# Kernel tuning notes

Measured on AMD Instinct MI355X. Metric: run time of the kernel, lower is better.

Reference implementation:

```python
import jax, jax.numpy as jnp
import numpy as np

# regular 3x3 kernel grid: row0 = dy (i-1), row1 = dx (j-1), k = 3*i + j
RY = jnp.array([-1., -1., -1., 0., 0., 0., 1., 1., 1.], dtype=jnp.float32)
RX = jnp.array([-1., 0., 1., -1., 0., 1., -1., 0., 1.], dtype=jnp.float32)


def conv2d(x, w, b):
    # 3x3, stride 1, pad 1, NCHW/OIHW
    out = jax.lax.conv_general_dilated(
        x, w, window_strides=(1, 1), padding=((1, 1), (1, 1)),
        dimension_numbers=('NCHW', 'OIHW', 'NCHW'))
    return out + b[None, :, None, None]


def group_norm(x, gamma, beta, num_groups, eps=1e-5):
    N, C, H, W = x.shape
    xg = x.reshape(N, num_groups, C // num_groups, H, W)
    mu = xg.mean(axis=(2, 3, 4), keepdims=True)
    var = xg.var(axis=(2, 3, 4), keepdims=True)
    xn = ((xg - mu) * jax.lax.rsqrt(var + eps)).reshape(N, C, H, W)
    return xn * gamma[None, :, None, None] + beta[None, :, None, None]


def build_offset(tm, tr):
    # tm: [N,4,H,W] per-pixel 2x2 affine [[m00,m01],[m10,m11]]; tr: [N,2,H,W] (ty, tx)
    m00, m01, m10, m11 = tm[:, 0], tm[:, 1], tm[:, 2], tm[:, 3]  # [N,H,W]
    ry = RY[None, :, None, None]
    rx = RX[None, :, None, None]
    # offset = M @ R - R, plus translation broadcast to all 9 points
    dy = m00[:, None] * ry + m01[:, None] * rx - ry + tr[:, 0:1]  # [N,9,H,W]
    dx = m10[:, None] * ry + m11[:, None] * rx - rx + tr[:, 1:2]  # [N,9,H,W]
    return dy, dx


def bilinear_sample(img, py, px):
    # img: [N,C,H,W]; py, px: [N,K,H,W] sampling locations; zero padding outside
    N, C, H, W = img.shape
    K = py.shape[1]
    y0f = jnp.floor(py)
    x0f = jnp.floor(px)
    wy1 = py - y0f
    wx1 = px - x0f
    wy0 = 1.0 - wy1
    wx0 = 1.0 - wx1
    y0 = y0f.astype(jnp.int32)
    x0 = x0f.astype(jnp.int32)
    img_flat = img.reshape(N, C, H * W)

    def gather(yi, xi):
        valid = ((yi >= 0) & (yi < H) & (xi >= 0) & (xi < W)).astype(img.dtype)
        idx = jnp.clip(yi, 0, H - 1) * W + jnp.clip(xi, 0, W - 1)  # [N,K,H,W]
        flat = idx.reshape(N, 1, K * H * W)
        vals = jnp.take_along_axis(img_flat, jnp.broadcast_to(flat, (N, C, K * H * W)), axis=2)
        return vals.reshape(N, C, K, H, W) * valid[:, None]

    v00 = gather(y0, x0)
    v01 = gather(y0, x0 + 1)
    v10 = gather(y0 + 1, x0)
    v11 = gather(y0 + 1, x0 + 1)
    return (v00 * (wy0 * wx0)[:, None] + v01 * (wy0 * wx1)[:, None]
            + v10 * (wy1 * wx0)[:, None] + v11 * (wy1 * wx1)[:, None])


def deform_conv(x, dy, dx, w, pad=1, dil=1):
    # x: [N,Cin,H,W]; dy,dx: [N,9,H,W]; w: [Cout,Cin,3,3]; stride 1
    N, C, H, W = x.shape
    k = jnp.arange(9)
    ki = (k // 3).astype(x.dtype)[None, :, None, None]
    kj = (k % 3).astype(x.dtype)[None, :, None, None]
    hh = jnp.arange(H, dtype=x.dtype)[None, None, :, None]
    ww = jnp.arange(W, dtype=x.dtype)[None, None, None, :]
    py = hh - pad + dil * ki + dy  # [N,9,H,W]
    px = ww - pad + dil * kj + dx
    sampled = bilinear_sample(x, py, px)  # [N,C,9,H,W]
    return jnp.einsum('nckhw,ock->nohw', sampled, w.reshape(w.shape[0], C, 9))


def setup_inputs() -> dict:
    key = jax.random.key(0)
    ks = jax.random.split(key, 16)
    N, C, H, W = 4, 256, 64, 64
    x = jax.random.normal(ks[0], (N, C, H, W), jnp.float32)
    def p(k, shape, s):
        return jax.random.normal(k, shape, jnp.float32) * s
    s_off = 0.01                       # small STN heads -> modest offsets
    s_dc = 1.0 / np.sqrt(C * 9.0)      # deform-conv fan-in init
    return {
        'x': x,
        'w_tm1': p(ks[1], (4, C, 3, 3), s_off), 'b_tm1': jnp.zeros((4,), jnp.float32),
        'w_tr1': p(ks[2], (2, C, 3, 3), s_off), 'b_tr1': jnp.zeros((2,), jnp.float32),
        'w_dc1': p(ks[3], (C, C, 3, 3), s_dc),
        'g1': jnp.ones((C,), jnp.float32), 'be1': jnp.zeros((C,), jnp.float32),
        'w_tm2': p(ks[4], (4, C, 3, 3), s_off), 'b_tm2': jnp.zeros((4,), jnp.float32),
        'w_tr2': p(ks[5], (2, C, 3, 3), s_off), 'b_tr2': jnp.zeros((2,), jnp.float32),
        'w_dc2': p(ks[6], (C, C, 3, 3), s_dc),
        'g2': jnp.ones((C,), jnp.float32), 'be2': jnp.zeros((C,), jnp.float32),
    }


def reference(x, w_tm1, b_tm1, w_tr1, b_tr1, w_dc1, g1, be1,
              w_tm2, b_tm2, w_tr2, b_tr2, w_dc2, g2, be2):
    GROUPS = 32
    residual = x
    dy1, dx1 = build_offset(conv2d(x, w_tm1, b_tm1), conv2d(x, w_tr1, b_tr1))
    out = deform_conv(x, dy1, dx1, w_dc1)
    out = jax.nn.relu(group_norm(out, g1, be1, GROUPS))
    dy2, dx2 = build_offset(conv2d(out, w_tm2, b_tm2), conv2d(out, w_tr2, b_tr2))
    out = deform_conv(out, dy2, dx2, w_dc2)
    out = group_norm(out, g2, be2, GROUPS)
    return jax.nn.relu(out + residual)
```

## Files before the change

### kernel.cpp

```cpp
#include <hip/hip_runtime.h>


typedef unsigned int u32;
typedef unsigned short u16;
typedef __attribute__((ext_vector_type(8))) short bf16x8;
typedef __attribute__((ext_vector_type(4))) float floatx4;

#define HW 4096
#define CHW 1048576

static __device__ __forceinline__ float bf2f(u16 u) {
    union { u32 i; float f; } c; c.i = ((u32)u) << 16; return c.f;
}
static __device__ __forceinline__ u16 f2bf(float f) {
    union { float f; u32 i; } c; c.f = f;
    u32 x = c.i;
    return (u16)((x + 0x7FFFu + ((x >> 16) & 1u)) >> 16);
}
static __device__ __forceinline__ u32 cvtpk(float a, float b) {
    u32 r;
    asm("v_cvt_pk_bf16_f32 %0, %1, %2" : "=v"(r) : "v"(a), "v"(b));
    return r;
}
static __device__ __forceinline__ void lbar() {
    __builtin_amdgcn_sched_barrier(0);
    asm volatile("s_waitcnt lgkmcnt(0)" ::: "memory");
    __builtin_amdgcn_s_barrier();
    __builtin_amdgcn_sched_barrier(0);
}
static __device__ __forceinline__ float loadv(const void* p, long i, int f32) {
    return f32 ? ((const float*)p)[i] : bf2f(((const u16*)p)[i]);
}
static __device__ __forceinline__ int sniff_f32(const u32* __restrict__ xw) {
    int cnt = 0;
    #pragma unroll
    for (int s = 0; s < 16; ++s) {
        union { u32 i; float f; } c;
        c.i = xw[s * 131 + 7];
        float a = fabsf(c.f);
        if (a > 1e-8f && a < 1e4f) ++cnt;
    }
    return (cnt >= 8) ? 1 : 0;
}

__global__ __launch_bounds__(256) void k_prep_all(
    const void* __restrict__ x,
    const void* __restrict__ wdc1, const void* __restrict__ wdc2,
    const void* __restrict__ wtm1, const void* __restrict__ wtr1,
    const void* __restrict__ wtm2, const void* __restrict__ wtr2,
    u16* __restrict__ xT, u16* __restrict__ wTg1, u16* __restrict__ wTg2,
    u16* __restrict__ wT61, u16* __restrict__ wT62)
{
    __shared__ u16 T[64 * 258];
    const int f32 = sniff_f32((const u32*)x);
    const int b = blockIdx.x;
    const int tid = threadIdx.x;

    if (b < 256) {
        const int n = b >> 6, h = b & 63;
        const long sb = (long)n * CHW + (h << 6);
        const int cb = tid >> 3;
        const int w0 = (tid & 7) << 3;
        if (f32) {
            const float* xp = (const float*)x;
            for (int it = 0; it < 8; ++it) {
                int c = (it << 5) + cb;
                const float* pr = xp + sb + (long)c * HW + w0;
                float4 a = ((const float4*)pr)[0];
                float4 d = ((const float4*)pr)[1];
                T[(w0 + 0) * 258 + c] = f2bf(a.x);
                T[(w0 + 1) * 258 + c] = f2bf(a.y);
                T[(w0 + 2) * 258 + c] = f2bf(a.z);
                T[(w0 + 3) * 258 + c] = f2bf(a.w);
                T[(w0 + 4) * 258 + c] = f2bf(d.x);
                T[(w0 + 5) * 258 + c] = f2bf(d.y);
                T[(w0 + 6) * 258 + c] = f2bf(d.z);
                T[(w0 + 7) * 258 + c] = f2bf(d.w);
            }
        } else {
            const u16* xp = (const u16*)x;
            for (int it = 0; it < 8; ++it) {
                int c = (it << 5) + cb;
                uint4 v = *(const uint4*)(xp + sb + (long)c * HW + w0);
                u32 ws[4] = {v.x, v.y, v.z, v.w};
                #pragma unroll
                for (int q = 0; q < 4; ++q) {
                    T[(w0 + 2 * q + 0) * 258 + c] = (u16)(ws[q] & 0xFFFFu);
                    T[(w0 + 2 * q + 1) * 258 + c] = (u16)(ws[q] >> 16);
                }
            }
        }
        __syncthreads();
        const int w = tid >> 2, cq = tid & 3;
        const u32* Tr = (const u32*)T;
        u16* ob = xT + (long)n * CHW + (long)((h << 6) + w) * 256 + cq * 64;
        #pragma unroll
        for (int s = 0; s < 8; ++s) {
            uint4 o;
            o.x = Tr[129 * w + 32 * cq + 4 * s + 0];
            o.y = Tr[129 * w + 32 * cq + 4 * s + 1];
            o.z = Tr[129 * w + 32 * cq + 4 * s + 2];
            o.w = Tr[129 * w + 32 * cq + 4 * s + 3];
            *(uint4*)&ob[s * 8] = o;
        }
    } else if (b < 2560) {
        const int r2 = (b >= 1408);
        const void* wdc = r2 ? wdc2 : wdc1;
        u16* wTg = r2 ? wTg2 : wTg1;
        int idx2 = (b - (r2 ? 1408 : 256)) * 256 + tid;
        int cp = idx2 & 15;
        int o  = (idx2 >> 4) & 255;
        int q  = idx2 >> 12;
        int k  = q >> 3;
        int c0 = ((q & 7) << 5) + (cp << 1);
        long s0 = (long)o * 2304 + c0 * 9 + k;
        ((u32*)wTg)[idx2] = cvtpk(loadv(wdc, s0, f32), loadv(wdc, s0 + 9, f32));
    } else {
        const int r2 = (b >= 2704);
        const void* wtm = r2 ? wtm2 : wtm1;
        const void* wtr = r2 ? wtr2 : wtr1;
        u16* wT6 = r2 ? wT62 : wT61;
        int i = (b - (r2 ? 2704 : 2560)) * 256 + tid;
        int q  = i >> 9;
        int o  = (i >> 5) & 15;
        int cc = i & 31;
        int k  = q >> 3;
        int c  = ((q & 7) << 5) + cc;
        float v = 0.f;
        if (o < 4)      v = loadv(wtm, (long)o * 2304 + c * 9 + k, f32);
        else if (o < 6) v = loadv(wtr, (long)(o - 4) * 2304 + c * 9 + k, f32);
        wT6[i] = f2bf(v);
    }
}

__global__ __launch_bounds__(512, 4) void k_deform(
    const u16* __restrict__ srcT, const u16* __restrict__ wTg,
    const u16* __restrict__ wT6,
    const void* __restrict__ b_tm, const void* __restrict__ b_tr,
    const u32* __restrict__ xw,
    u16* __restrict__ raw, float* __restrict__ pstats)
{
    __shared__ float red[8][32][17];
    __shared__ float tl[6 * 32];
    __shared__ __align__(16) u32 Sl[2][4096];
    __shared__ int   g_y0[288];
    __shared__ int   g_x0[288];
    __shared__ float g_wy[288];
    __shared__ float g_wx[288];

    const int tid = threadIdx.x;
    const int bid = blockIdx.x;
    const int n = bid >> 7, h = (bid >> 1) & 63, half = bid & 1;
    const int wb = half << 5;
    const int lane = tid & 63;
    const int quad = lane >> 4;
    const int l16  = lane & 15;
    const int wv   = tid >> 6;
    const long nbase = (long)n * CHW;
    const u16* sp = srcT + nbase;

    {
        floatx4 acc6[2];
        acc6[0] = (floatx4){0.f, 0.f, 0.f, 0.f};
        acc6[1] = (floatx4){0.f, 0.f, 0.f, 0.f};
        for (int qi = 0; qi < 9; ++qi) {
            const int q = wv * 9 + qi;
            const int k = q >> 3, cb = q & 7;
            const int ky = k / 3, kx = k % 3;
            const int row = h + ky - 1;
            const bool rv = (row >= 0) && (row < 64);
            bf16x8 av = *(const bf16x8*)&wT6[(((q << 4) + l16) << 5) + (quad << 3)];
            #pragma unroll
            for (int j = 0; j < 2; ++j) {
                int psrc = wb + (j << 4) + l16 + kx - 1;
                bf16x8 bv = {0, 0, 0, 0, 0, 0, 0, 0};
                if (rv && psrc >= 0 && psrc < 64)
                    bv = *(const bf16x8*)&sp[(((long)(row << 6) + psrc) << 8) + (cb << 5) + (quad << 3)];
                acc6[j] = __builtin_amdgcn_mfma_f32_16x16x32_bf16(av, bv, acc6[j], 0, 0, 0);
            }
        }
        #pragma unroll
        for (int j = 0; j < 2; ++j)
            #pragma unroll
            for (int r = 0; r < 4; ++r)
                red[wv][(j << 4) + l16][(quad << 2) + r] = acc6[j][r];
        __syncthreads();
        if (tid < 192) {
            const int o = tid >> 5, px = tid & 31;
            float s = 0.f;
            #pragma unroll
            for (int v = 0; v < 8; ++v) s += red[v][px][o];
            const int f32 = sniff_f32(xw);
            float bias = (o < 4) ? loadv(b_tm, o, f32) : loadv(b_tr, o - 4, f32);
            tl[o * 32 + px] = s + bias;
        }
        __syncthreads();
    }

    for (int i = tid; i < 288; i += 512) {
        int k = i >> 5, ww2 = i & 31;
        float m00 = tl[ww2],       m01 = tl[32 + ww2];
        float m10 = tl[64 + ww2],  m11 = tl[96 + ww2];
        float tr0 = tl[128 + ww2], tr1 = tl[160 + ww2];
        float ry = (float)(k / 3) - 1.f;
        float rx = (float)(k % 3) - 1.f;
        float dy = m00 * ry + m01 * rx - ry + tr0;
        float dx = m10 * ry + m11 * rx - rx + tr1;
        float py = (float)h + ry + dy;
        float px = (float)(wb + ww2) + rx + dx;
        float y0f = floorf(py), x0f = floorf(px);
        g_y0[i] = (int)y0f; g_x0[i] = (int)x0f;
        g_wy[i] = py - y0f; g_wx[i] = px - x0f;
    }
    __syncthreads();

    const int px   = tid >> 4;
    const int slot = tid & 15;
    const int o0   = wv << 5;
    const u32 xw_s = (u32)((px  & 7) << 2);
    const u32 xsw  = (u32)((l16 & 7) << 2);
    const u32 q4x  = (u32)(quad << 2);

    floatx4 acc[2][2];
    #pragma unroll
    for (int i = 0; i < 2; ++i)
        #pragma unroll
        for (int j = 0; j < 2; ++j)
            acc[i][j] = (floatx4){0.f, 0.f, 0.f, 0.f};

    const int wlane = ((o0 + l16) << 5) + (quad << 3);
    const u16* wq = wTg;

    const u16 *p00, *p01, *p10, *p11;
    float cw00, cw01, cw10, cw11;

    auto mkptr = [&](int k) {
        int gi = (k << 5) + px;
        int y0 = g_y0[gi], x0 = g_x0[gi];
        int yc0 = min(max(y0, 0), 63),     yc1 = min(max(y0 + 1, 0), 63);
        int xc0 = min(max(x0, 0), 63),     xc1 = min(max(x0 + 1, 0), 63);
        const u16* bp = sp + (slot << 3);
        p00 = bp + (((yc0 << 6) + xc0) << 8);
        p01 = bp + (((yc0 << 6) + xc1) << 8);
        p10 = bp + (((yc1 << 6) + xc0) << 8);
        p11 = bp + (((yc1 << 6) + xc1) << 8);
    };
    auto mkcw = [&](int k) {
        int gi = (k << 5) + px;
        int y0 = g_y0[gi], x0 = g_x0[gi];
        float wy1 = g_wy[gi], wx1 = g_wx[gi];
        float wy0 = 1.f - wy1, wx0 = 1.f - wx1;
        bool yv0 = (y0 >= 0) && (y0 < 64);
        bool yv1 = (y0 >= -1) && (y0 < 63);
        bool xv0 = (x0 >= 0) && (x0 < 64);
        bool xv1 = (x0 >= -1) && (x0 < 63);
        cw00 = (yv0 && xv0) ? wy0 * wx0 : 0.f;
        cw01 = (yv0 && xv1) ? wy0 * wx1 : 0.f;
        cw10 = (yv1 && xv0) ? wy1 * wx0 : 0.f;
        cw11 = (yv1 && xv1) ? wy1 * wx1 : 0.f;
    };

    uint4 GA, GB, GC, GD, HA, HB, HC, HD;
    auto GATHER = [&]() {
        GA = *(const uint4*)(p00);  HA = *(const uint4*)(p00 + 128);
        GB = *(const uint4*)(p01);  HB = *(const uint4*)(p01 + 128);
        GC = *(const uint4*)(p10);  HC = *(const uint4*)(p10 + 128);
        GD = *(const uint4*)(p11);  HD = *(const uint4*)(p11 + 128);
    };

    bf16x8 W0[4], W1[4];
    auto WLD = [&](int s) {
        W0[s] = *(const bf16x8*)(wq + wlane);
        W1[s] = *(const bf16x8*)(wq + wlane + 512);
        wq += 8192;
    };
    auto MFMA4 = [&](int ws, bf16x8 b0, bf16x8 b1) {
        acc[0][0] = __builtin_amdgcn_mfma_f32_16x16x32_bf16(W0[ws], b0, acc[0][0], 0, 0, 0);
        acc[1][0] = __builtin_amdgcn_mfma_f32_16x16x32_bf16(W1[ws], b0, acc[1][0], 0, 0, 0);
        acc[0][1] = __builtin_amdgcn_mfma_f32_16x16x32_bf16(W0[ws], b1, acc[0][1], 0, 0, 0);
        acc[1][1] = __builtin_amdgcn_mfma_f32_16x16x32_bf16(W1[ws], b1, acc[1][1], 0, 0, 0);
    };

#define BIL(a, b, c, d) cvtpk( \
    fmaf(cw00, bf2f((u16)(a)), fmaf(cw01, bf2f((u16)(b)), \
    fmaf(cw10, bf2f((u16)(c)), cw11 * bf2f((u16)(d))))), \
    fmaf(cw00, bf2f((u16)((a) >> 16)), fmaf(cw01, bf2f((u16)((b) >> 16)), \
    fmaf(cw10, bf2f((u16)((c) >> 16)), cw11 * bf2f((u16)((d) >> 16))))))

    mkptr(0); GATHER();
    WLD(0); WLD(1);

    for (int k = 0; k < 9; ++k) {
        const int buf = k & 1;
        mkcw(k);
        uint4 v0 = make_uint4(BIL(GA.x, GB.x, GC.x, GD.x), BIL(GA.y, GB.y, GC.y, GD.y),
                              BIL(GA.z, GB.z, GC.z, GD.z), BIL(GA.w, GB.w, GC.w, GD.w));
        uint4 v1 = make_uint4(BIL(HA.x, HB.x, HC.x, HD.x), BIL(HA.y, HB.y, HC.y, HD.y),
                              BIL(HA.z, HB.z, HC.z, HD.z), BIL(HA.w, HB.w, HC.w, HD.w));
        u32* wp = &Sl[buf][((u32)(px << 7)) + (((u32)(slot << 2)) ^ xw_s)];
        *(uint4*)wp = v0;
        *(uint4*)(wp + 64) = v1;
        if (k < 8) { mkptr(k + 1); GATHER(); }
        lbar();
        const u32* sb = &Sl[buf][0];
        #pragma unroll
        for (int c = 0; c < 8; ++c) {
            const u32 offc = (((u32)(c << 4)) | q4x) ^ xsw;
            bf16x8 b0 = *(const bf16x8*)(sb + ((u32)(l16 << 7)) + offc);
            bf16x8 b1 = *(const bf16x8*)(sb + ((u32)((16 + l16) << 7)) + offc);
            if (k < 8 || c < 6) WLD((c + 2) & 3);
            MFMA4(c & 3, b0, b1);
        }
    }
#undef BIL

    #pragma unroll
    for (int i = 0; i < 2; ++i) {
        float s1 = 0.f, s2 = 0.f;
        #pragma unroll
        for (int j = 0; j < 2; ++j)
            #pragma unroll
            for (int r = 0; r < 4; ++r) {
                float v = acc[i][j][r];
                s1 += v; s2 += v * v;
            }
        #pragma unroll
        for (int off = 1; off <= 16; off <<= 1) {
            s1 += __shfl_xor(s1, off, 64);
            s2 += __shfl_xor(s2, off, 64);
        }
        if ((lane & 31) == 0) {
            int g = (o0 >> 3) + 2 * i + (lane >> 5);
            pstats[((long)bid << 6) + (g << 1)]     = s1;
            pstats[((long)bid << 6) + (g << 1) + 1] = s2;
        }
    }

    #pragma unroll
    for (int i = 0; i < 2; ++i)
        #pragma unroll
        for (int j = 0; j < 2; ++j)
            #pragma unroll
            for (int r = 0; r < 4; ++r) {
                int o = o0 + i * 16 + quad * 4 + r;
                raw[nbase + ((long)o << 12) + (h << 6) + wb + (j << 4) + l16]
                    = f2bf(acc[i][j][r]);
            }
}

__global__ __launch_bounds__(256) void k_gn_relu(
    const u16* __restrict__ raw, const float* __restrict__ pstats,
    const void* __restrict__ gamma, const void* __restrict__ beta,
    const u32* __restrict__ xw,
    u16* __restrict__ out1)
{
    __shared__ u16 T[64 * 258];
    __shared__ float sred[4][64];
    __shared__ float sl[64];
    const int f32 = sniff_f32(xw);
    const int bid = blockIdx.x;
    const int n = bid >> 6, h = bid & 63;
    const int tid = threadIdx.x;

    {
        const int v = tid & 63, part = tid >> 6;
        float a = 0.f;
        for (int j = part * 32; j < part * 32 + 32; ++j)
            a += pstats[(((long)n * 128 + j) << 6) + v];
        sred[part][v] = a;
        __syncthreads();
        if (tid < 64) sl[tid] = sred[0][tid] + sred[1][tid] + sred[2][tid] + sred[3][tid];
        __syncthreads();
    }

    const u16* rb = raw + (long)n * CHW + (h << 6);
    const int cb = tid >> 3;
    const int w0 = (tid & 7) << 3;
    for (int it = 0; it < 8; ++it) {
        int c = (it << 5) + cb;
        int g = c >> 3;
        float mean = sl[g * 2] * (1.f / 32768.f);
        float var  = sl[g * 2 + 1] * (1.f / 32768.f) - mean * mean;
        float rstd = rsqrtf(var + 1e-5f);
        float ga = loadv(gamma, c, f32) * rstd;
        float be = loadv(beta, c, f32) - mean * ga;
        uint4 v = *(const uint4*)(rb + (long)c * HW + w0);
        u32 ws[4] = {v.x, v.y, v.z, v.w};
        #pragma unroll
        for (int q = 0; q < 4; ++q) {
            float a = fmaxf(fmaf(bf2f((u16)(ws[q] & 0xFFFFu)), ga, be), 0.f);
            float b = fmaxf(fmaf(bf2f((u16)(ws[q] >> 16)),     ga, be), 0.f);
            T[(w0 + 2 * q + 0) * 258 + c] = f2bf(a);
            T[(w0 + 2 * q + 1) * 258 + c] = f2bf(b);
        }
    }
    __syncthreads();
    const int w = tid >> 2, cq = tid & 3;
    const u32* Tr = (const u32*)T;
    u16* ob = out1 + (long)n * CHW + (long)((h << 6) + w) * 256 + cq * 64;
    #pragma unroll
    for (int s = 0; s < 8; ++s) {
        uint4 o;
        o.x = Tr[129 * w + 32 * cq + 4 * s + 0];
        o.y = Tr[129 * w + 32 * cq + 4 * s + 1];
        o.z = Tr[129 * w + 32 * cq + 4 * s + 2];
        o.w = Tr[129 * w + 32 * cq + 4 * s + 3];
        *(uint4*)&ob[s * 8] = o;
    }
}

__global__ __launch_bounds__(256) void k_gn_final(
    const u16* __restrict__ raw, const float* __restrict__ pstats,
    const void* __restrict__ gamma, const void* __restrict__ beta,
    const void* __restrict__ x,
    void* __restrict__ outp)
{
    __shared__ float rr[256];
    const int f32 = sniff_f32((const u32*)x);
    const int tid = threadIdx.x;
    const long e0 = ((long)blockIdx.x) << 11;
    const int n = (int)(e0 >> 20);
    const int c0 = (int)((e0 >> 12) & 255);
    const int g = c0 >> 3;

    {
        int j = tid & 127, sv = tid >> 7;
        rr[tid] = pstats[(((long)n * 128 + j) << 6) + (g << 1) + sv];
        __syncthreads();
        #pragma unroll
        for (int s = 64; s >= 1; s >>= 1) {
            if ((tid & 127) < s) rr[tid] += rr[tid + s];
            __syncthreads();
        }
    }
    float mean = rr[0] * (1.f / 32768.f);
    float var  = rr[128] * (1.f / 32768.f) - mean * mean;
    float rstd = rsqrtf(var + 1e-5f);

    const long i = blockIdx.x * 256 + tid;
    const long e = i << 3;
    const int c = (int)((e >> 12) & 255);
    float ga = loadv(gamma, c, f32) * rstd;
    float be = loadv(beta, c, f32) - mean * ga;
    uint4 p = ((const uint4*)raw)[i];
    u32 ww[4] = {p.x, p.y, p.z, p.w};
    float v[8];
    #pragma unroll
    for (int q = 0; q < 4; ++q) {
        v[2 * q + 0] = fmaxf(fmaf(bf2f((u16)(ww[q] & 0xFFFFu)), ga, be) + loadv(x, e + 2 * q + 0, f32), 0.f);
        v[2 * q + 1] = fmaxf(fmaf(bf2f((u16)(ww[q] >> 16)),     ga, be) + loadv(x, e + 2 * q + 1, f32), 0.f);
    }
    if (f32) {
        float4* op = (float4*)((float*)outp + e);
        op[0] = make_float4(v[0], v[1], v[2], v[3]);
        op[1] = make_float4(v[4], v[5], v[6], v[7]);
    } else {
        uint4 o;
        o.x = cvtpk(v[0], v[1]);
        o.y = cvtpk(v[2], v[3]);
        o.z = cvtpk(v[4], v[5]);
        o.w = cvtpk(v[6], v[7]);
        ((uint4*)outp)[i] = o;
    }
}

extern "C" void kernel_launch(void* const* d_in, const int* in_sizes, int n_in,
                              void* d_out, int out_size, void* d_ws, size_t ws_size,
                              hipStream_t stream) {
    const void* x     = d_in[0];
    const void* w_tm1 = d_in[1];
    const void* b_tm1 = d_in[2];
    const void* w_tr1 = d_in[3];
    const void* b_tr1 = d_in[4];
    const void* w_dc1 = d_in[5];
    const void* g1    = d_in[6];
    const void* be1   = d_in[7];
    const void* w_tm2 = d_in[8];
    const void* b_tm2 = d_in[9];
    const void* w_tr2 = d_in[10];
    const void* b_tr2 = d_in[11];
    const void* w_dc2 = d_in[12];
    const void* g2    = d_in[13];
    const void* be2   = d_in[14];

    char* wsb = (char*)d_ws;
    u16*   xT     = (u16*)wsb;
    u16*   raw    = (u16*)(wsb + 8388608);
    u16*   wTg1   = (u16*)(wsb + 16777216);
    u16*   wTg2   = (u16*)(wsb + 17956864);
    u16*   wT61   = (u16*)(wsb + 19136512);
    u16*   wT62   = (u16*)(wsb + 19210240);
    float* pstats = (float*)(wsb + 19283968);
    u16*   out1   = xT;
    const u32* xw = (const u32*)x;

    k_prep_all<<<2848, 256, 0, stream>>>(x, w_dc1, w_dc2, w_tm1, w_tr1, w_tm2, w_tr2,
                                         xT, wTg1, wTg2, wT61, wT62);
    k_deform  <<<512, 512, 0, stream>>>(xT, wTg1, wT61, b_tm1, b_tr1, xw, raw, pstats);
    k_gn_relu <<<256, 256, 0, stream>>>(raw, pstats, g1, be1, xw, out1);
    k_deform  <<<512, 512, 0, stream>>>(out1, wTg2, wT62, b_tm2, b_tr2, xw, raw, pstats);
    k_gn_final<<<2048, 256, 0, stream>>>(raw, pstats, g2, be2, x, d_out);
}
```

Measured before the change: 239.6 us.

## Process full image rows per deform block with 16 waves instead of half rows

Each deformable-conv block now covers a whole 64-pixel row with 1024 threads (16 waves, 16 output channels each) instead of half a row with 512 threads. The idea is to share the bilinear-gathered tile across more output channels and halve the grid, so offset-conv rows and gathers are not done twice per row. The stats layout shrinks to 64 partials per image and the GN kernels are updated to match. In exchange, shared memory use doubles to about 64 KB, only 256 blocks launch (roughly one per CU), and only 8 of 16 waves take part in the offset conv.

Measured after the change: 221.6 us. 7.5% less time.

```diff
diff --git a/kernel.cpp b/kernel.cpp
--- a/kernel.cpp
+++ b/kernel.cpp
@@ -133,25 +133,23 @@
     }
 }
 
-__global__ __launch_bounds__(512, 4) void k_deform(
+__global__ __launch_bounds__(1024, 4) void k_deform(
     const u16* __restrict__ srcT, const u16* __restrict__ wTg,
     const u16* __restrict__ wT6,
     const void* __restrict__ b_tm, const void* __restrict__ b_tr,
     const u32* __restrict__ xw,
     u16* __restrict__ raw, float* __restrict__ pstats)
 {
-    __shared__ float red[8][32][17];
-    __shared__ float tl[6 * 32];
-    __shared__ __align__(16) u32 Sl[2][4096];
-    __shared__ int   g_y0[288];
-    __shared__ int   g_x0[288];
-    __shared__ float g_wy[288];
-    __shared__ float g_wx[288];
+    __shared__ __align__(16) char shm[65536];
+    __shared__ float tl[6 * 64];
+    __shared__ int   g_y0[576];
+    __shared__ int   g_x0[576];
+    __shared__ float g_wy[576];
+    __shared__ float g_wx[576];
 
     const int tid = threadIdx.x;
     const int bid = blockIdx.x;
-    const int n = bid >> 7, h = (bid >> 1) & 63, half = bid & 1;
-    const int wb = half << 5;
+    const int n = bid >> 6, h = bid & 63;
     const int lane = tid & 63;
     const int quad = lane >> 4;
     const int l16  = lane & 15;
@@ -160,54 +158,58 @@
     const u16* sp = srcT + nbase;
 
     {
-        floatx4 acc6[2];
-        acc6[0] = (floatx4){0.f, 0.f, 0.f, 0.f};
-        acc6[1] = (floatx4){0.f, 0.f, 0.f, 0.f};
-        for (int qi = 0; qi < 9; ++qi) {
-            const int q = wv * 9 + qi;
-            const int k = q >> 3, cb = q & 7;
-            const int ky = k / 3, kx = k % 3;
-            const int row = h + ky - 1;
-            const bool rv = (row >= 0) && (row < 64);
-            bf16x8 av = *(const bf16x8*)&wT6[(((q << 4) + l16) << 5) + (quad << 3)];
+        float (*red)[64][17] = (float (*)[64][17])shm;
+        if (wv < 8) {
+            floatx4 acc6[4];
             #pragma unroll
-            for (int j = 0; j < 2; ++j) {
-                int psrc = wb + (j << 4) + l16 + kx - 1;
-                bf16x8 bv = {0, 0, 0, 0, 0, 0, 0, 0};
-                if (rv && psrc >= 0 && psrc < 64)
-                    bv = *(const bf16x8*)&sp[(((long)(row << 6) + psrc) << 8) + (cb << 5) + (quad << 3)];
-                acc6[j] = __builtin_amdgcn_mfma_f32_16x16x32_bf16(av, bv, acc6[j], 0, 0, 0);
+            for (int j = 0; j < 4; ++j) acc6[j] = (floatx4){0.f, 0.f, 0.f, 0.f};
+            for (int qi = 0; qi < 9; ++qi) {
+                const int q = wv * 9 + qi;
+                const int k = q >> 3, cb = q & 7;
+                const int ky = k / 3, kx = k % 3;
+                const int row = h + ky - 1;
+                const bool rv = (row >= 0) && (row < 64);
+                bf16x8 av = *(const bf16x8*)&wT6[(((q << 4) + l16) << 5) + (quad << 3)];
+                #pragma unroll
+                for (int j = 0; j < 4; ++j) {
+                    int psrc = (j << 4) + l16 + kx - 1;
+                    bf16x8 bv = {0, 0, 0, 0, 0, 0, 0, 0};
+                    if (rv && psrc >= 0 && psrc < 64)
+                        bv = *(const bf16x8*)&sp[(((long)(row << 6) + psrc) << 8) + (cb << 5) + (quad << 3)];
+                    acc6[j] = __builtin_amdgcn_mfma_f32_16x16x32_bf16(av, bv, acc6[j], 0, 0, 0);
+                }
             }
-        }
-        #pragma unroll
-        for (int j = 0; j < 2; ++j)
             #pragma unroll
-            for (int r = 0; r < 4; ++r)
-                red[wv][(j << 4) + l16][(quad << 2) + r] = acc6[j][r];
+            for (int j = 0; j < 4; ++j)
+                #pragma unroll
+                for (int r = 0; r < 4; ++r)
+                    red[wv][(j << 4) + l16][(quad << 2) + r] = acc6[j][r];
+        }
         __syncthreads();
-        if (tid < 192) {
-            const int o = tid >> 5, px = tid & 31;
+        if (tid < 384) {
+            const int o = tid >> 6, px = tid & 63;
             float s = 0.f;
             #pragma unroll
             for (int v = 0; v < 8; ++v) s += red[v][px][o];
             const int f32 = sniff_f32(xw);
             float bias = (o < 4) ? loadv(b_tm, o, f32) : loadv(b_tr, o - 4, f32);
-            tl[o * 32 + px] = s + bias;
+            tl[o * 64 + px] = s + bias;
         }
         __syncthreads();
     }
 
-    for (int i = tid; i < 288; i += 512) {
-        int k = i >> 5, ww2 = i & 31;
-        float m00 = tl[ww2],       m01 = tl[32 + ww2];
-        float m10 = tl[64 + ww2],  m11 = tl[96 + ww2];
-        float tr0 = tl[128 + ww2], tr1 = tl[160 + ww2];
+    if (tid < 576) {
+        int i = tid;
+        int k = i >> 6, ww2 = i & 63;
+        float m00 = tl[ww2],        m01 = tl[64 + ww2];
+        float m10 = tl[128 + ww2],  m11 = tl[192 + ww2];
+        float tr0 = tl[256 + ww2],  tr1 = tl[320 + ww2];
         float ry = (float)(k / 3) - 1.f;
         float rx = (float)(k % 3) - 1.f;
         float dy = m00 * ry + m01 * rx - ry + tr0;
         float dx = m10 * ry + m11 * rx - rx + tr1;
         float py = (float)h + ry + dy;
-        float px = (float)(wb + ww2) + rx + dx;
+        float px = (float)ww2 + rx + dx;
         float y0f = floorf(py), x0f = floorf(px);
         g_y0[i] = (int)y0f; g_x0[i] = (int)x0f;
         g_wy[i] = py - y0f; g_wx[i] = px - x0f;
@@ -216,17 +218,16 @@
 
     const int px   = tid >> 4;
     const int slot = tid & 15;
-    const int o0   = wv << 5;
+    const int o0   = wv << 4;
     const u32 xw_s = (u32)((px  & 7) << 2);
     const u32 xsw  = (u32)((l16 & 7) << 2);
     const u32 q4x  = (u32)(quad << 2);
 
-    floatx4 acc[2][2];
+    u32* Sl = (u32*)shm;
+
+    floatx4 acc[4];
     #pragma unroll
-    for (int i = 0; i < 2; ++i)
-        #pragma unroll
-        for (int j = 0; j < 2; ++j)
-            acc[i][j] = (floatx4){0.f, 0.f, 0.f, 0.f};
+    for (int g = 0; g < 4; ++g) acc[g] = (floatx4){0.f, 0.f, 0.f, 0.f};
 
     const int wlane = ((o0 + l16) << 5) + (quad << 3);
     const u16* wq = wTg;
@@ -235,7 +236,7 @@
     float cw00, cw01, cw10, cw11;
 
     auto mkptr = [&](int k) {
-        int gi = (k << 5) + px;
+        int gi = (k << 6) + px;
         int y0 = g_y0[gi], x0 = g_x0[gi];
         int yc0 = min(max(y0, 0), 63),     yc1 = min(max(y0 + 1, 0), 63);
         int xc0 = min(max(x0, 0), 63),     xc1 = min(max(x0 + 1, 0), 63);
@@ -246,7 +247,7 @@
         p11 = bp + (((yc1 << 6) + xc1) << 8);
     };
     auto mkcw = [&](int k) {
-        int gi = (k << 5) + px;
+        int gi = (k << 6) + px;
         int y0 = g_y0[gi], x0 = g_x0[gi];
         float wy1 = g_wy[gi], wx1 = g_wx[gi];
         float wy0 = 1.f - wy1, wx0 = 1.f - wx1;
@@ -268,17 +269,10 @@
         GD = *(const uint4*)(p11);  HD = *(const uint4*)(p11 + 128);
     };
 
-    bf16x8 W0[4], W1[4];
+    bf16x8 W[4];
     auto WLD = [&](int s) {
-        W0[s] = *(const bf16x8*)(wq + wlane);
-        W1[s] = *(const bf16x8*)(wq + wlane + 512);
+        W[s] = *(const bf16x8*)(wq + wlane);
         wq += 8192;
-    };
-    auto MFMA4 = [&](int ws, bf16x8 b0, bf16x8 b1) {
-        acc[0][0] = __builtin_amdgcn_mfma_f32_16x16x32_bf16(W0[ws], b0, acc[0][0], 0, 0, 0);
-        acc[1][0] = __builtin_amdgcn_mfma_f32_16x16x32_bf16(W1[ws], b0, acc[1][0], 0, 0, 0);
-        acc[0][1] = __builtin_amdgcn_mfma_f32_16x16x32_bf16(W0[ws], b1, acc[0][1], 0, 0, 0);
-        acc[1][1] = __builtin_amdgcn_mfma_f32_16x16x32_bf16(W1[ws], b1, acc[1][1], 0, 0, 0);
     };
 
 #define BIL(a, b, c, d) cvtpk( \
@@ -297,31 +291,36 @@
                               BIL(GA.z, GB.z, GC.z, GD.z), BIL(GA.w, GB.w, GC.w, GD.w));
         uint4 v1 = make_uint4(BIL(HA.x, HB.x, HC.x, HD.x), BIL(HA.y, HB.y, HC.y, HD.y),
                               BIL(HA.z, HB.z, HC.z, HD.z), BIL(HA.w, HB.w, HC.w, HD.w));
-        u32* wp = &Sl[buf][((u32)(px << 7)) + (((u32)(slot << 2)) ^ xw_s)];
+        u32* wp = &Sl[((u32)(buf << 13)) + ((u32)(px << 7)) + (((u32)(slot << 2)) ^ xw_s)];
         *(uint4*)wp = v0;
         *(uint4*)(wp + 64) = v1;
         if (k < 8) { mkptr(k + 1); GATHER(); }
         lbar();
-        const u32* sb = &Sl[buf][0];
+        const u32* sb = &Sl[(u32)(buf << 13)];
         #pragma unroll
         for (int c = 0; c < 8; ++c) {
             const u32 offc = (((u32)(c << 4)) | q4x) ^ xsw;
-            bf16x8 b0 = *(const bf16x8*)(sb + ((u32)(l16 << 7)) + offc);
+            bf16x8 b0 = *(const bf16x8*)(sb + ((u32)(( 0 + l16) << 7)) + offc);
             bf16x8 b1 = *(const bf16x8*)(sb + ((u32)((16 + l16) << 7)) + offc);
+            bf16x8 b2 = *(const bf16x8*)(sb + ((u32)((32 + l16) << 7)) + offc);
+            bf16x8 b3 = *(const bf16x8*)(sb + ((u32)((48 + l16) << 7)) + offc);
             if (k < 8 || c < 6) WLD((c + 2) & 3);
-            MFMA4(c & 3, b0, b1);
+            const int ws = c & 3;
+            acc[0] = __builtin_amdgcn_mfma_f32_16x16x32_bf16(W[ws], b0, acc[0], 0, 0, 0);
+            acc[1] = __builtin_amdgcn_mfma_f32_16x16x32_bf16(W[ws], b1, acc[1], 0, 0, 0);
+            acc[2] = __builtin_amdgcn_mfma_f32_16x16x32_bf16(W[ws], b2, acc[2], 0, 0, 0);
+            acc[3] = __builtin_amdgcn_mfma_f32_16x16x32_bf16(W[ws], b3, acc[3], 0, 0, 0);
         }
     }
 #undef BIL
 
-    #pragma unroll
-    for (int i = 0; i < 2; ++i) {
+    {
         float s1 = 0.f, s2 = 0.f;
         #pragma unroll
-        for (int j = 0; j < 2; ++j)
+        for (int g = 0; g < 4; ++g)
             #pragma unroll
             for (int r = 0; r < 4; ++r) {
-                float v = acc[i][j][r];
+                float v = acc[g][r];
                 s1 += v; s2 += v * v;
             }
         #pragma unroll
@@ -330,22 +329,20 @@
             s2 += __shfl_xor(s2, off, 64);
         }
         if ((lane & 31) == 0) {
-            int g = (o0 >> 3) + 2 * i + (lane >> 5);
-            pstats[((long)bid << 6) + (g << 1)]     = s1;
-            pstats[((long)bid << 6) + (g << 1) + 1] = s2;
+            int gg = (o0 >> 3) + (lane >> 5);
+            pstats[((long)bid << 6) + (gg << 1)]     = s1;
+            pstats[((long)bid << 6) + (gg << 1) + 1] = s2;
         }
     }
 
     #pragma unroll
-    for (int i = 0; i < 2; ++i)
-        #pragma unroll
-        for (int j = 0; j < 2; ++j)
-            #pragma unroll
-            for (int r = 0; r < 4; ++r) {
-                int o = o0 + i * 16 + quad * 4 + r;
-                raw[nbase + ((long)o << 12) + (h << 6) + wb + (j << 4) + l16]
-                    = f2bf(acc[i][j][r]);
-            }
+    for (int g = 0; g < 4; ++g)
+        #pragma unroll
+        for (int r = 0; r < 4; ++r) {
+            int o = o0 + quad * 4 + r;
+            raw[nbase + ((long)o << 12) + (h << 6) + (g << 4) + l16]
+                = f2bf(acc[g][r]);
+        }
 }
 
 __global__ __launch_bounds__(256) void k_gn_relu(
@@ -365,8 +362,8 @@
     {
         const int v = tid & 63, part = tid >> 6;
         float a = 0.f;
-        for (int j = part * 32; j < part * 32 + 32; ++j)
-            a += pstats[(((long)n * 128 + j) << 6) + v];
+        for (int j = part * 16; j < part * 16 + 16; ++j)
+            a += pstats[(((long)n * 64 + j) << 6) + v];
         sred[part][v] = a;
         __syncthreads();
         if (tid < 64) sl[tid] = sred[0][tid] + sred[1][tid] + sred[2][tid] + sred[3][tid];
@@ -425,7 +422,7 @@
 
     {
         int j = tid & 127, sv = tid >> 7;
-        rr[tid] = pstats[(((long)n * 128 + j) << 6) + (g << 1) + sv];
+        rr[tid] = (j < 64) ? pstats[(((long)n * 64 + j) << 6) + (g << 1) + sv] : 0.f;
         __syncthreads();
         #pragma unroll
         for (int s = 64; s >= 1; s >>= 1) {
@@ -496,8 +493,8 @@
 
     k_prep_all<<<2848, 256, 0, stream>>>(x, w_dc1, w_dc2, w_tm1, w_tr1, w_tm2, w_tr2,
                                          xT, wTg1, wTg2, wT61, wT62);
-    k_deform  <<<512, 512, 0, stream>>>(xT, wTg1, wT61, b_tm1, b_tr1, xw, raw, pstats);
+    k_deform  <<<256, 1024, 0, stream>>>(xT, wTg1, wT61, b_tm1, b_tr1, xw, raw, pstats);
     k_gn_relu <<<256, 256, 0, stream>>>(raw, pstats, g1, be1, xw, out1);
-    k_deform  <<<512, 512, 0, stream>>>(out1, wTg2, wT62, b_tm2, b_tr2, xw, raw, pstats);
+    k_deform  <<<256, 1024, 0, stream>>>(out1, wTg2, wT62, b_tm2, b_tr2, xw, raw, pstats);
     k_gn_final<<<2048, 256, 0, stream>>>(raw, pstats, g2, be2, x, d_out);
 }
```
